# Kernel optimization log

Hardware: AMD Instinct MI355X
Metric: run time of the kernel (lower is better)

The kernel has to match this reference:

```python
import jax, jax.numpy as jnp
import numpy as np

H = 8          # num_heads
D = 64         # head_dim
HID = 512      # hidden_size
W = 128        # window_size
NEG = -1e9

def setup_inputs() -> dict:
    key = jax.random.key(0)
    ks = jax.random.split(key, 12)
    B, S = 2, 2048
    def lin(i):
        w = jax.random.normal(ks[i], (HID, HID), dtype=jnp.float32) * (1.0 / np.sqrt(HID))
        b = jax.random.normal(ks[i + 1], (HID,), dtype=jnp.float32) * 0.01
        return w, b
    Wq, bq = lin(0)
    Wk, bk = lin(2)
    Wv, bv = lin(4)
    Wo, bo = lin(6)
    return {
        "value": jax.random.normal(ks[8], (B, S, HID), dtype=jnp.float32),
        "key": jax.random.normal(ks[9], (B, S, HID), dtype=jnp.float32),
        "query": jax.random.normal(ks[10], (B, S, HID), dtype=jnp.float32),
        "Wq": Wq, "bq": bq, "Wk": Wk, "bk": bk,
        "Wv": Wv, "bv": bv, "Wo": Wo, "bo": bo,
    }

def reference(value, key, query, Wq, bq, Wk, bk, Wv, bv, Wo, bo):
    B, S, _ = query.shape
    def heads(x, Wt, b):
        # torch Linear: x @ W.T + b ; then [B,S,H,D] -> [B,H,S,D]
        return (x @ Wt.T + b).reshape(B, S, H, D).transpose(0, 2, 1, 3)
    Q = heads(query, Wq, bq)
    K = heads(key, Wk, bk)
    V = heads(value, Wv, bv)
    scores = jnp.einsum('bhqd,bhkd->bhqk', Q, K) / jnp.sqrt(jnp.float32(D))
    idx = jnp.arange(S)
    local = jnp.abs(idx[:, None] - idx[None, :]) <= W  # [S,S] band mask
    scores = jnp.where(local[None, None], scores, NEG)
    weights = jax.nn.softmax(scores, axis=-1)
    out = jnp.einsum('bhqk,bhkd->bhqd', weights, V)
    out = out.transpose(0, 2, 1, 3).reshape(B, S, HID)
    return out @ Wo.T + bo
```

## Files before the change

kernel.cpp:

```cpp
#include <hip/hip_runtime.h>
#include <stdint.h>

#define B_   2
#define S_   2048
#define H_   8
#define D_   64
#define HID_ 512
#define W_   128
#define M_   (B_ * S_)
#define E_   (M_ * HID_)
#define PPAD_ 72
#define M0_  12.0f

typedef unsigned short u16;
typedef __attribute__((ext_vector_type(8))) __bf16 bf16x8;
typedef __attribute__((ext_vector_type(4))) float  floatx4;

__device__ __forceinline__ u16 f2b(float f) {
    union { float f; unsigned int i; } x;
    x.f = f;
    unsigned int r = x.i + 0x7FFFu + ((x.i >> 16) & 1u);
    return (u16)(r >> 16);
}

__device__ __forceinline__ void cvt8_store(float4 a, float4 b, u16* dst) {
    bf16x8 v;
    v[0] = (__bf16)a.x; v[1] = (__bf16)a.y; v[2] = (__bf16)a.z; v[3] = (__bf16)a.w;
    v[4] = (__bf16)b.x; v[5] = (__bf16)b.y; v[6] = (__bf16)b.z; v[7] = (__bf16)b.w;
    *(bf16x8*)dst = v;
}

__device__ __forceinline__ void mfma_tile(const u16* As, const u16* Bs,
                                          int wave, int r16, int quad,
                                          floatx4 acc[4][4]) {
    bf16x8 a0[4], b[4];
#pragma unroll
    for (int t = 0; t < 4; t++) {
        a0[t] = *(const bf16x8*)&As[(wave * 64 + t * 16 + r16) * 32 + quad * 8];
        b[t]  = *(const bf16x8*)&Bs[(t * 16 + r16) * 32 + quad * 8];
    }
#pragma unroll
    for (int i = 0; i < 4; i++)
#pragma unroll
        for (int j = 0; j < 4; j++)
            acc[i][j] = __builtin_amdgcn_mfma_f32_16x16x32_bf16(a0[i], b[j], acc[i][j], 0, 0, 0);
}

template <int MODE>
__device__ __forceinline__ void gemm_fp32in_body(
    const float* __restrict__ Xf, const float* __restrict__ Wf,
    const float* __restrict__ bias, u16* __restrict__ outH) {
    __shared__ u16 As[2][128 * 32];
    __shared__ u16 Bs[2][64 * 32];

    const int tid  = threadIdx.x;
    const int wave = tid >> 6;
    const int lane = tid & 63;
    const int r16  = lane & 15;
    const int quad = lane >> 4;
    const int m0 = blockIdx.x * 128;
    const int n0 = blockIdx.y * 64;
    const int m_base = m0 + wave * 64;

    const int ar  = tid >> 2;
    const int ak  = (tid & 3) * 8;
    const int br  = tid >> 1;
    const int bk2 = (tid & 1) * 16;

    floatx4 zero = {0.f, 0.f, 0.f, 0.f};
    floatx4 acc[4][4];
#pragma unroll
    for (int i = 0; i < 4; i++)
#pragma unroll
        for (int j = 0; j < 4; j++) acc[i][j] = zero;

    float4 rA0[8], rB0[4], rA1[8], rB1[4];

#define LOADT(rA, rB, k0) do {                                                 \
        _Pragma("unroll")                                                      \
        for (int e = 0; e < 4; e++) {                                          \
            const float4* s_ = (const float4*)(Xf + (size_t)(m0 + e * 32 + ar) * HID_ + (k0) + ak); \
            rA[2 * e] = s_[0]; rA[2 * e + 1] = s_[1];                          \
        }                                                                      \
        const float4* w_ = (const float4*)(Wf + (size_t)(n0 + br) * HID_ + (k0) + bk2); \
        rB[0] = w_[0]; rB[1] = w_[1]; rB[2] = w_[2]; rB[3] = w_[3];            \
    } while (0)
#define STORET(rA, rB, buf) do {                                               \
        _Pragma("unroll")                                                      \
        for (int e = 0; e < 4; e++)                                            \
            cvt8_store(rA[2 * e], rA[2 * e + 1], &As[buf][(e * 32 + ar) * 32 + ak]); \
        cvt8_store(rB[0], rB[1], &Bs[buf][br * 32 + bk2]);                     \
        cvt8_store(rB[2], rB[3], &Bs[buf][br * 32 + bk2 + 8]);                 \
    } while (0)

    LOADT(rA0, rB0, 0);
    LOADT(rA1, rB1, 32);
    STORET(rA0, rB0, 0);
    __syncthreads();

    for (int t = 0; t < 16; t += 2) {
        if (t + 2 < 16) LOADT(rA0, rB0, (t + 2) * 32);
        mfma_tile(As[0], Bs[0], wave, r16, quad, acc);
        STORET(rA1, rB1, 1);
        __syncthreads();
        if (t + 3 < 16) LOADT(rA1, rB1, (t + 3) * 32);
        mfma_tile(As[1], Bs[1], wave, r16, quad, acc);
        if (t + 2 < 16) STORET(rA0, rB0, 0);
        __syncthreads();
    }
#undef LOADT
#undef STORET

    const int bb = m_base >> 11;
    if (MODE == 1) {
#pragma unroll
        for (int j = 0; j < 4; j++) {
            const int col = n0 + j * 16 + r16;
            const int h = col >> 6, d = col & (D_ - 1);
            const float bv = bias[col];
            const size_t base = (size_t)(bb * H_ + h) * S_;
#pragma unroll
            for (int i = 0; i < 4; i++)
#pragma unroll
                for (int r = 0; r < 4; r++) {
                    const int s = (m_base & (S_ - 1)) + i * 16 + quad * 4 + r;
                    outH[(base + s) * D_ + d] = f2b(acc[i][j][r] + bv);
                }
        }
    } else {
#pragma unroll
        for (int j = 0; j < 4; j++) {
            const int col = n0 + j * 16 + r16;
            const int h = col >> 6, d = col & (D_ - 1);
            const float bv = bias[col];
            const size_t base = ((size_t)(bb * H_ + h) * D_ + d) * S_;
            const int s0 = (m_base & (S_ - 1)) + quad * 4;
#pragma unroll
            for (int i = 0; i < 4; i++) {
                ushort4 hs;
                hs.x = f2b(acc[i][j][0] + bv);
                hs.y = f2b(acc[i][j][1] + bv);
                hs.z = f2b(acc[i][j][2] + bv);
                hs.w = f2b(acc[i][j][3] + bv);
                *(ushort4*)(outH + base + s0 + i * 16) = hs;
            }
        }
    }
}

__global__ __launch_bounds__(128) void qkv_fused_kernel(
    const float* __restrict__ xq, const float* __restrict__ xk, const float* __restrict__ xv,
    const float* __restrict__ wq, const float* __restrict__ wk, const float* __restrict__ wv,
    const float* __restrict__ bq, const float* __restrict__ bk, const float* __restrict__ bv,
    u16* __restrict__ P) {
    if (blockIdx.z == 0)      gemm_fp32in_body<1>(xq, wq, bq, P);
    else if (blockIdx.z == 1) gemm_fp32in_body<1>(xk, wk, bk, P + E_);
    else                      gemm_fp32in_body<2>(xv, wv, bv, P + 2 * (size_t)E_);
}

__global__ __launch_bounds__(128) void out_fused_kernel(
    const u16* __restrict__ AOh, const float* __restrict__ Wf,
    const float* __restrict__ bias, float* __restrict__ outF) {
    __shared__ u16 As[2][128 * 32];
    __shared__ u16 Bs[2][64 * 32];

    const int tid  = threadIdx.x;
    const int wave = tid >> 6;
    const int lane = tid & 63;
    const int r16  = lane & 15;
    const int quad = lane >> 4;
    const int m0 = blockIdx.x * 128;
    const int n0 = blockIdx.y * 64;
    const int m_base = m0 + wave * 64;

    const int ar  = tid >> 2;
    const int ak  = (tid & 3) * 8;
    const int br  = tid >> 1;
    const int bk2 = (tid & 1) * 16;

    floatx4 zero = {0.f, 0.f, 0.f, 0.f};
    floatx4 acc[4][4];
#pragma unroll
    for (int i = 0; i < 4; i++)
#pragma unroll
        for (int j = 0; j < 4; j++) acc[i][j] = zero;

    uint4  rA0[4], rA1[4];
    float4 rB0[4], rB1[4];

#define LOADO(rA, rB, k0) do {                                                 \
        _Pragma("unroll")                                                      \
        for (int e = 0; e < 4; e++)                                            \
            rA[e] = *(const uint4*)(AOh + (size_t)(m0 + e * 32 + ar) * HID_ + (k0) + ak); \
        const float4* w_ = (const float4*)(Wf + (size_t)(n0 + br) * HID_ + (k0) + bk2); \
        rB[0] = w_[0]; rB[1] = w_[1]; rB[2] = w_[2]; rB[3] = w_[3];            \
    } while (0)
#define STOREO(rA, rB, buf) do {                                               \
        _Pragma("unroll")                                                      \
        for (int e = 0; e < 4; e++)                                            \
            *(uint4*)&As[buf][(e * 32 + ar) * 32 + ak] = rA[e];                \
        cvt8_store(rB[0], rB[1], &Bs[buf][br * 32 + bk2]);                     \
        cvt8_store(rB[2], rB[3], &Bs[buf][br * 32 + bk2 + 8]);                 \
    } while (0)

    LOADO(rA0, rB0, 0);
    LOADO(rA1, rB1, 32);
    STOREO(rA0, rB0, 0);
    __syncthreads();

    for (int t = 0; t < 16; t += 2) {
        if (t + 2 < 16) LOADO(rA0, rB0, (t + 2) * 32);
        mfma_tile(As[0], Bs[0], wave, r16, quad, acc);
        STOREO(rA1, rB1, 1);
        __syncthreads();
        if (t + 3 < 16) LOADO(rA1, rB1, (t + 3) * 32);
        mfma_tile(As[1], Bs[1], wave, r16, quad, acc);
        if (t + 2 < 16) STOREO(rA0, rB0, 0);
        __syncthreads();
    }
#undef LOADO
#undef STOREO

#pragma unroll
    for (int j = 0; j < 4; j++) {
        const int col = n0 + j * 16 + r16;
        const float bv = bias[col];
#pragma unroll
        for (int i = 0; i < 4; i++) {
            const int row0 = m_base + i * 16 + quad * 4;
#pragma unroll
            for (int r = 0; r < 4; r++)
                outF[(size_t)(row0 + r) * HID_ + col] = acc[i][j][r] + bv;
        }
    }
}

__global__ __launch_bounds__(256) void attn_kernel(
    const u16* __restrict__ Qh, const u16* __restrict__ Kh,
    const u16* __restrict__ Vth, u16* __restrict__ AOh) {
    __shared__ u16 Ps[4][16][PPAD_];
    __shared__ u16 Osh[4][16][PPAD_];

    const int tid  = threadIdx.x;
    const int wave = tid >> 6;
    const int lane = tid & 63;
    const int r16 = lane & 15, quad = lane >> 4;
    const int qt = blockIdx.x, bh = blockIdx.y;
    const int q0 = qt * 64 + wave * 16;
    const size_t sd = (size_t)bh * S_ * D_;
    const size_t ds = (size_t)bh * D_ * S_;

    bf16x8 qf[2];
#pragma unroll
    for (int ks = 0; ks < 2; ks++)
        qf[ks] = *(const bf16x8*)(Qh + sd + (size_t)(q0 + r16) * D_ + ks * 32 + quad * 8);

    floatx4 zero = {0.f, 0.f, 0.f, 0.f};
    floatx4 O[4];
    float lsum[4];
#pragma unroll
    for (int j = 0; j < 4; j++) O[j] = zero;
#pragma unroll
    for (int r = 0; r < 4; r++) lsum[r] = 0.f;

    int t_lo = qt - 2; if (t_lo < 0) t_lo = 0;
    int t_hi = qt + 2; if (t_hi > S_ / 64 - 1) t_hi = S_ / 64 - 1;

    for (int t = t_lo; t <= t_hi; ++t) {
        const int k0 = t * 64;
        floatx4 sa[4];
#pragma unroll
        for (int j = 0; j < 4; j++) sa[j] = zero;

#pragma unroll
        for (int ks = 0; ks < 2; ks++) {
            bf16x8 kf[4];
#pragma unroll
            for (int j = 0; j < 4; j++)
                kf[j] = *(const bf16x8*)(Kh + sd + (size_t)(k0 + j * 16 + r16) * D_ + ks * 32 + quad * 8);
#pragma unroll
            for (int j = 0; j < 4; j++)
                sa[j] = __builtin_amdgcn_mfma_f32_16x16x32_bf16(qf[ks], kf[j], sa[j], 0, 0, 0);
        }

#pragma unroll
        for (int j = 0; j < 4; j++) {
            const int kc = k0 + j * 16 + r16;
#pragma unroll
            for (int r = 0; r < 4; r++) {
                const int q = q0 + quad * 4 + r;
                const bool valid = (unsigned)(kc - q + W_) <= (unsigned)(2 * W_);
                const float p = valid ? __expf(fmaf(sa[j][r], 0.125f, -M0_)) : 0.f;
                lsum[r] += p;
                Ps[wave][quad * 4 + r][j * 16 + r16] = f2b(p);
            }
        }

#pragma unroll
        for (int ks = 0; ks < 2; ks++) {
            bf16x8 pf = *(const bf16x8*)&Ps[wave][r16][ks * 32 + quad * 8];
#pragma unroll
            for (int j = 0; j < 4; j++) {
                bf16x8 vf = *(const bf16x8*)(Vth + ds + (size_t)(j * 16 + r16) * S_ + k0 + ks * 32 + quad * 8);
                O[j] = __builtin_amdgcn_mfma_f32_16x16x32_bf16(pf, vf, O[j], 0, 0, 0);
            }
        }
    }

#pragma unroll
    for (int r = 0; r < 4; r++) {
        float l = lsum[r];
#pragma unroll
        for (int off = 1; off < 16; off <<= 1) l += __shfl_xor(l, off, 64);
        lsum[r] = l;
    }

#pragma unroll
    for (int r = 0; r < 4; r++) {
        const float linv = 1.f / lsum[r];
#pragma unroll
        for (int j = 0; j < 4; j++)
            Osh[wave][quad * 4 + r][j * 16 + r16] = f2b(O[j][r] * linv);
    }

    const int b = bh >> 3, h = bh & 7;
    const int qq = lane >> 2;
    const int d0 = (lane & 3) * 16;
    u16* dst = AOh + (size_t)(b * S_ + q0 + qq) * HID_ + h * D_ + d0;
    *(uint4*)dst       = *(const uint4*)&Osh[wave][qq][d0];
    *(uint4*)(dst + 8) = *(const uint4*)&Osh[wave][qq][d0 + 8];
}

extern "C" void kernel_launch(void* const* d_in, const int* in_sizes, int n_in,
                              void* d_out, int out_size, void* d_ws, size_t ws_size,
                              hipStream_t stream) {
    const float* value = (const float*)d_in[0];
    const float* key_  = (const float*)d_in[1];
    const float* query = (const float*)d_in[2];
    const float* Wq = (const float*)d_in[3];
    const float* bq = (const float*)d_in[4];
    const float* Wk = (const float*)d_in[5];
    const float* bk = (const float*)d_in[6];
    const float* Wv = (const float*)d_in[7];
    const float* bv = (const float*)d_in[8];
    const float* Wo = (const float*)d_in[9];
    const float* bo = (const float*)d_in[10];

    u16* P   = (u16*)d_ws;
    u16* AOh = P + 3 * (size_t)E_;

    qkv_fused_kernel<<<dim3(M_ / 128, HID_ / 64, 3), 128, 0, stream>>>(
        query, key_, value, Wq, Wk, Wv, bq, bk, bv, P);
    attn_kernel<<<dim3(S_ / 64, B_ * H_), 256, 0, stream>>>(
        P, P + E_, P + 2 * (size_t)E_, AOh);
    out_fused_kernel<<<dim3(M_ / 128, HID_ / 64), 128, 0, stream>>>(
        AOh, Wo, bo, (float*)d_out);
}
```

Before: 143.2 us.

## Pre-convert inputs to bf16 and stage GEMM tiles via direct global-to-LDS loads

Adds a separate conversion kernel that turns the fp32 activations and weights into bf16 in workspace. The QKV and output GEMMs then share one bf16 body that loads 64-wide K tiles straight into XOR-swizzled LDS with global_load_lds, in place of register staging with in-kernel conversion. The goal is to cut per-tile conversion work and register pressure and to avoid LDS bank conflicts. In exchange it adds an extra launch and a full fp32 read plus bf16 write pass over the inputs, and drops the double-buffered prefetch in favour of a single buffer with two barriers per step.

```diff
diff --git a/kernel.cpp b/kernel.cpp
--- a/kernel.cpp
+++ b/kernel.cpp
@@ -9,6 +9,7 @@
 #define W_   128
 #define M_   (B_ * S_)
 #define E_   (M_ * HID_)
+#define WSZ_ (HID_ * HID_)
 #define PPAD_ 72
 #define M0_  12.0f
 
@@ -17,10 +18,15 @@
 typedef __attribute__((ext_vector_type(4))) float  floatx4;
 
 __device__ __forceinline__ u16 f2b(float f) {
-    union { float f; unsigned int i; } x;
-    x.f = f;
-    unsigned int r = x.i + 0x7FFFu + ((x.i >> 16) & 1u);
-    return (u16)(r >> 16);
+    union { __bf16 b; u16 u; } x;
+    x.b = (__bf16)f;
+    return x.u;
+}
+
+__device__ __forceinline__ void gll16(const u16* g, u16* l) {
+    __builtin_amdgcn_global_load_lds(
+        (const __attribute__((address_space(1))) unsigned int*)g,
+        (__attribute__((address_space(3))) unsigned int*)l, 16, 0, 0);
 }
 
 __device__ __forceinline__ void cvt8_store(float4 a, float4 b, u16* dst) {
@@ -30,28 +36,35 @@
     *(bf16x8*)dst = v;
 }
 
-__device__ __forceinline__ void mfma_tile(const u16* As, const u16* Bs,
-                                          int wave, int r16, int quad,
-                                          floatx4 acc[4][4]) {
-    bf16x8 a0[4], b[4];
-#pragma unroll
-    for (int t = 0; t < 4; t++) {
-        a0[t] = *(const bf16x8*)&As[(wave * 64 + t * 16 + r16) * 32 + quad * 8];
-        b[t]  = *(const bf16x8*)&Bs[(t * 16 + r16) * 32 + quad * 8];
-    }
-#pragma unroll
-    for (int i = 0; i < 4; i++)
-#pragma unroll
-        for (int j = 0; j < 4; j++)
-            acc[i][j] = __builtin_amdgcn_mfma_f32_16x16x32_bf16(a0[i], b[j], acc[i][j], 0, 0, 0);
+__global__ __launch_bounds__(256) void cvt_kernel(
+    const float* __restrict__ q, const float* __restrict__ k, const float* __restrict__ v,
+    const float* __restrict__ wq, const float* __restrict__ wk,
+    const float* __restrict__ wv, const float* __restrict__ wo,
+    u16* __restrict__ ws) {
+    const int seg = blockIdx.y;
+    const float* src; u16* dst; int n;
+    switch (seg) {
+        case 0:  src = q;  dst = ws + 4 * (size_t)E_;            n = E_;   break;
+        case 1:  src = k;  dst = ws + 5 * (size_t)E_;            n = E_;   break;
+        case 2:  src = v;  dst = ws + 6 * (size_t)E_;            n = E_;   break;
+        case 3:  src = wq; dst = ws + 7 * (size_t)E_;            n = WSZ_; break;
+        case 4:  src = wk; dst = ws + 7 * (size_t)E_ + WSZ_;     n = WSZ_; break;
+        case 5:  src = wv; dst = ws + 7 * (size_t)E_ + 2 * WSZ_; n = WSZ_; break;
+        default: src = wo; dst = ws + 7 * (size_t)E_ + 3 * WSZ_; n = WSZ_; break;
+    }
+    const int i = (blockIdx.x * 256 + threadIdx.x) * 8;
+    if (i >= n) return;
+    const float4* s = (const float4*)(src + i);
+    cvt8_store(s[0], s[1], dst + i);
 }
 
 template <int MODE>
-__device__ __forceinline__ void gemm_fp32in_body(
-    const float* __restrict__ Xf, const float* __restrict__ Wf,
-    const float* __restrict__ bias, u16* __restrict__ outH) {
-    __shared__ u16 As[2][128 * 32];
-    __shared__ u16 Bs[2][64 * 32];
+__device__ __forceinline__ void gemm_bf16_body(
+    const u16* __restrict__ Ah, const u16* __restrict__ Bh,
+    const float* __restrict__ bias, u16* __restrict__ outH,
+    float* __restrict__ outF) {
+    __shared__ u16 As[128 * 64];
+    __shared__ u16 Bs[64 * 64];
 
     const int tid  = threadIdx.x;
     const int wave = tid >> 6;
@@ -62,11 +75,6 @@
     const int n0 = blockIdx.y * 64;
     const int m_base = m0 + wave * 64;
 
-    const int ar  = tid >> 2;
-    const int ak  = (tid & 3) * 8;
-    const int br  = tid >> 1;
-    const int bk2 = (tid & 1) * 16;
-
     floatx4 zero = {0.f, 0.f, 0.f, 0.f};
     floatx4 acc[4][4];
 #pragma unroll
@@ -74,42 +82,51 @@
 #pragma unroll
         for (int j = 0; j < 4; j++) acc[i][j] = zero;
 
-    float4 rA0[8], rB0[4], rA1[8], rB1[4];
-
-#define LOADT(rA, rB, k0) do {                                                 \
-        _Pragma("unroll")                                                      \
-        for (int e = 0; e < 4; e++) {                                          \
-            const float4* s_ = (const float4*)(Xf + (size_t)(m0 + e * 32 + ar) * HID_ + (k0) + ak); \
-            rA[2 * e] = s_[0]; rA[2 * e + 1] = s_[1];                          \
-        }                                                                      \
-        const float4* w_ = (const float4*)(Wf + (size_t)(n0 + br) * HID_ + (k0) + bk2); \
-        rB[0] = w_[0]; rB[1] = w_[1]; rB[2] = w_[2]; rB[3] = w_[3];            \
-    } while (0)
-#define STORET(rA, rB, buf) do {                                               \
-        _Pragma("unroll")                                                      \
-        for (int e = 0; e < 4; e++)                                            \
-            cvt8_store(rA[2 * e], rA[2 * e + 1], &As[buf][(e * 32 + ar) * 32 + ak]); \
-        cvt8_store(rB[0], rB[1], &Bs[buf][br * 32 + bk2]);                     \
-        cvt8_store(rB[2], rB[3], &Bs[buf][br * 32 + bk2 + 8]);                 \
-    } while (0)
-
-    LOADT(rA0, rB0, 0);
-    LOADT(rA1, rB1, 32);
-    STORET(rA0, rB0, 0);
-    __syncthreads();
-
-    for (int t = 0; t < 16; t += 2) {
-        if (t + 2 < 16) LOADT(rA0, rB0, (t + 2) * 32);
-        mfma_tile(As[0], Bs[0], wave, r16, quad, acc);
-        STORET(rA1, rB1, 1);
+    int aoff[2], boff[2];
+#pragma unroll
+    for (int ks = 0; ks < 2; ks++) {
+        const int sw = (((ks * 4 + quad) ^ (r16 & 7)) * 8);
+        aoff[ks] = (wave * 64 + r16) * 64 + sw;
+        boff[ks] = r16 * 64 + sw;
+    }
+
+    for (int k0 = 0; k0 < HID_; k0 += 64) {
+#pragma unroll
+        for (int e = 0; e < 8; e++) {
+            const int li = (wave * 8 + e) * 64 + lane;
+            const int r  = li >> 3;
+            const int cl = (li & 7) ^ (r & 7);
+            gll16(Ah + (size_t)(m0 + r) * HID_ + k0 + cl * 8,
+                  As + (size_t)(wave * 8 + e) * 512);
+        }
+#pragma unroll
+        for (int e = 0; e < 4; e++) {
+            const int li = (wave * 4 + e) * 64 + lane;
+            const int r  = li >> 3;
+            const int cl = (li & 7) ^ (r & 7);
+            gll16(Bh + (size_t)(n0 + r) * HID_ + k0 + cl * 8,
+                  Bs + (size_t)(wave * 4 + e) * 512);
+        }
         __syncthreads();
-        if (t + 3 < 16) LOADT(rA1, rB1, (t + 3) * 32);
-        mfma_tile(As[1], Bs[1], wave, r16, quad, acc);
-        if (t + 2 < 16) STORET(rA0, rB0, 0);
+
+        bf16x8 af[2][4], bf[2][4];
+#pragma unroll
+        for (int ks = 0; ks < 2; ks++)
+#pragma unroll
+            for (int t = 0; t < 4; t++) {
+                af[ks][t] = *(const bf16x8*)&As[aoff[ks] + t * 1024];
+                bf[ks][t] = *(const bf16x8*)&Bs[boff[ks] + t * 1024];
+            }
+#pragma unroll
+        for (int ks = 0; ks < 2; ks++)
+#pragma unroll
+            for (int i = 0; i < 4; i++)
+#pragma unroll
+                for (int j = 0; j < 4; j++)
+                    acc[i][j] = __builtin_amdgcn_mfma_f32_16x16x32_bf16(
+                        af[ks][i], bf[ks][j], acc[i][j], 0, 0, 0);
         __syncthreads();
     }
-#undef LOADT
-#undef STORET
 
     const int bb = m_base >> 11;
     if (MODE == 1) {
@@ -127,7 +144,7 @@
                     outH[(base + s) * D_ + d] = f2b(acc[i][j][r] + bv);
                 }
         }
-    } else {
+    } else if (MODE == 2) {
 #pragma unroll
         for (int j = 0; j < 4; j++) {
             const int col = n0 + j * 16 + r16;
@@ -145,94 +162,43 @@
                 *(ushort4*)(outH + base + s0 + i * 16) = hs;
             }
         }
-    }
-}
-
-__global__ __launch_bounds__(128) void qkv_fused_kernel(
-    const float* __restrict__ xq, const float* __restrict__ xk, const float* __restrict__ xv,
-    const float* __restrict__ wq, const float* __restrict__ wk, const float* __restrict__ wv,
+    } else {
+#pragma unroll
+        for (int j = 0; j < 4; j++) {
+            const int col = n0 + j * 16 + r16;
+            const float bv = bias[col];
+#pragma unroll
+            for (int i = 0; i < 4; i++) {
+                const int row0 = m_base + i * 16 + quad * 4;
+#pragma unroll
+                for (int r = 0; r < 4; r++)
+                    outF[(size_t)(row0 + r) * HID_ + col] = acc[i][j][r] + bv;
+            }
+        }
+    }
+}
+
+__global__ __launch_bounds__(128) void qkv_kernel(
+    const u16* __restrict__ ws,
     const float* __restrict__ bq, const float* __restrict__ bk, const float* __restrict__ bv,
     u16* __restrict__ P) {
-    if (blockIdx.z == 0)      gemm_fp32in_body<1>(xq, wq, bq, P);
-    else if (blockIdx.z == 1) gemm_fp32in_body<1>(xk, wk, bk, P + E_);
-    else                      gemm_fp32in_body<2>(xv, wv, bv, P + 2 * (size_t)E_);
-}
-
-__global__ __launch_bounds__(128) void out_fused_kernel(
-    const u16* __restrict__ AOh, const float* __restrict__ Wf,
+    const u16* X; const u16* Wt; const float* bias; u16* out;
+    if (blockIdx.z == 0) {
+        X = ws + 4 * (size_t)E_; Wt = ws + 7 * (size_t)E_;            bias = bq; out = P;
+        gemm_bf16_body<1>(X, Wt, bias, out, nullptr);
+    } else if (blockIdx.z == 1) {
+        X = ws + 5 * (size_t)E_; Wt = ws + 7 * (size_t)E_ + WSZ_;     bias = bk; out = P + E_;
+        gemm_bf16_body<1>(X, Wt, bias, out, nullptr);
+    } else {
+        X = ws + 6 * (size_t)E_; Wt = ws + 7 * (size_t)E_ + 2 * WSZ_; bias = bv; out = P + 2 * (size_t)E_;
+        gemm_bf16_body<2>(X, Wt, bias, out, nullptr);
+    }
+}
+
+__global__ __launch_bounds__(128) void out_kernel(
+    const u16* __restrict__ AOh, const u16* __restrict__ Woh,
     const float* __restrict__ bias, float* __restrict__ outF) {
-    __shared__ u16 As[2][128 * 32];
-    __shared__ u16 Bs[2][64 * 32];
-
-    const int tid  = threadIdx.x;
-    const int wave = tid >> 6;
-    const int lane = tid & 63;
-    const int r16  = lane & 15;
-    const int quad = lane >> 4;
-    const int m0 = blockIdx.x * 128;
-    const int n0 = blockIdx.y * 64;
-    const int m_base = m0 + wave * 64;
-
-    const int ar  = tid >> 2;
-    const int ak  = (tid & 3) * 8;
-    const int br  = tid >> 1;
-    const int bk2 = (tid & 1) * 16;
-
-    floatx4 zero = {0.f, 0.f, 0.f, 0.f};
-    floatx4 acc[4][4];
-#pragma unroll
-    for (int i = 0; i < 4; i++)
-#pragma unroll
-        for (int j = 0; j < 4; j++) acc[i][j] = zero;
-
-    uint4  rA0[4], rA1[4];
-    float4 rB0[4], rB1[4];
-
-#define LOADO(rA, rB, k0) do {                                                 \
-        _Pragma("unroll")                                                      \
-        for (int e = 0; e < 4; e++)                                            \
-            rA[e] = *(const uint4*)(AOh + (size_t)(m0 + e * 32 + ar) * HID_ + (k0) + ak); \
-        const float4* w_ = (const float4*)(Wf + (size_t)(n0 + br) * HID_ + (k0) + bk2); \
-        rB[0] = w_[0]; rB[1] = w_[1]; rB[2] = w_[2]; rB[3] = w_[3];            \
-    } while (0)
-#define STOREO(rA, rB, buf) do {                                               \
-        _Pragma("unroll")                                                      \
-        for (int e = 0; e < 4; e++)                                            \
-            *(uint4*)&As[buf][(e * 32 + ar) * 32 + ak] = rA[e];                \
-        cvt8_store(rB[0], rB[1], &Bs[buf][br * 32 + bk2]);                     \
-        cvt8_store(rB[2], rB[3], &Bs[buf][br * 32 + bk2 + 8]);                 \
-    } while (0)
-
-    LOADO(rA0, rB0, 0);
-    LOADO(rA1, rB1, 32);
-    STOREO(rA0, rB0, 0);
-    __syncthreads();
-
-    for (int t = 0; t < 16; t += 2) {
-        if (t + 2 < 16) LOADO(rA0, rB0, (t + 2) * 32);
-        mfma_tile(As[0], Bs[0], wave, r16, quad, acc);
-        STOREO(rA1, rB1, 1);
-        __syncthreads();
-        if (t + 3 < 16) LOADO(rA1, rB1, (t + 3) * 32);
-        mfma_tile(As[1], Bs[1], wave, r16, quad, acc);
-        if (t + 2 < 16) STOREO(rA0, rB0, 0);
-        __syncthreads();
-    }
-#undef LOADO
-#undef STOREO
-
-#pragma unroll
-    for (int j = 0; j < 4; j++) {
-        const int col = n0 + j * 16 + r16;
-        const float bv = bias[col];
-#pragma unroll
-        for (int i = 0; i < 4; i++) {
-            const int row0 = m_base + i * 16 + quad * 4;
-#pragma unroll
-            for (int r = 0; r < 4; r++)
-                outF[(size_t)(row0 + r) * HID_ + col] = acc[i][j][r] + bv;
-        }
-    }
+    gemm_bf16_body<3>(AOh, Woh, bias, nullptr, outF);
 }
 
 __global__ __launch_bounds__(256) void attn_kernel(
@@ -346,13 +312,14 @@
     const float* Wo = (const float*)d_in[9];
     const float* bo = (const float*)d_in[10];
 
-    u16* P   = (u16*)d_ws;
-    u16* AOh = P + 3 * (size_t)E_;
-
-    qkv_fused_kernel<<<dim3(M_ / 128, HID_ / 64, 3), 128, 0, stream>>>(
-        query, key_, value, Wq, Wk, Wv, bq, bk, bv, P);
+    u16* ws  = (u16*)d_ws;
+    u16* P   = ws;
+    u16* AOh = ws + 3 * (size_t)E_;
+    u16* Woh = ws + 7 * (size_t)E_ + 3 * (size_t)WSZ_;
+
+    cvt_kernel<<<dim3(1024, 7), 256, 0, stream>>>(query, key_, value, Wq, Wk, Wv, Wo, ws);
+    qkv_kernel<<<dim3(M_ / 128, HID_ / 64, 3), 128, 0, stream>>>(ws, bq, bk, bv, P);
     attn_kernel<<<dim3(S_ / 64, B_ * H_), 256, 0, stream>>>(
         P, P + E_, P + 2 * (size_t)E_, AOh);
-    out_fused_kernel<<<dim3(M_ / 128, HID_ / 64), 128, 0, stream>>>(
-        AOh, Wo, bo, (float*)d_out);
-}
+    out_kernel<<<dim3(M_ / 128, HID_ / 64), 128, 0, stream>>>(AOh, Woh, bo, (float*)d_out);
+}
```

After: 139.2 us. 2.8% less time.
